# Optimization experiments

Hardware: AMD Instinct MI355X
Metric: run time of the kernel (lower is better)

## Reference

```python
import jax, jax.numpy as jnp
import numpy as np

B_, DIM, NPTS = 16, 128, 16384
J, K, L = 16, 128, 128   # kernel_mode, GkNN_mode_out, GkNN_mode_in
R, M1, M2 = 8, 64, 64    # low-rank A/B dims and mask modes


def setup_inputs() -> dict:
    key = jax.random.key(0)
    ks = jax.random.split(key, 9)
    scale = 1.0 / (L * K)
    return {
        "x": jax.random.normal(ks[0], (B_, DIM, NPTS), jnp.float32),
        "bases": jax.random.normal(ks[1], (NPTS, K), jnp.float32),
        "wbases": jax.random.normal(ks[2], (NPTS, L), jnp.float32),
        "product": jax.random.normal(ks[3], (K, L), jnp.float32),
        "D_out": jax.random.normal(ks[4], (J, K), jnp.float32),
        "D_in": jax.random.normal(ks[5], (J, L), jnp.float32),
        "A": jax.random.normal(ks[6], (J, R, M1), jnp.float32),
        "B": jax.random.normal(ks[7], (J, R, M2), jnp.float32),
        "weights": scale * jax.random.normal(ks[8], (DIM, DIM, J), jnp.float32),
    }


def reference(x, bases, wbases, product, D_out, D_in, A, B, weights):
    # project onto weighted bases: (b, c, npts) @ (npts, L) -> (b, c, L)
    x_hat = jnp.einsum('bcx,xl->bcl', x, wbases)
    # H tensor: (J, K, L) broadcast product + low-rank correction
    H = D_out[:, :, None] * D_in[:, None, :] * product[None, :, :]
    Q = jnp.einsum('jrm,jrn->jmn', A, B)  # bmm(A^T, B): (J, M1, M2)
    H = H.at[:, :Q.shape[1], :Q.shape[2]].add(Q)
    # mode mixing: (J,K,L) x (b,i,L) -> (b,i,J,K), then weights (i,o,J)
    x_hat1 = jnp.einsum('jkl,bil->bijk', H, x_hat)
    y = jnp.einsum('ioj,bijk->bok', weights, x_hat1)
    # back to physical space: (b, o, K) x (npts, K) -> (b, o, npts)
    return jnp.einsum('bok,xk->box', y, bases)
```

## Files before the change

### kernel.cpp

```cpp
#include <hip/hip_runtime.h>

#define B_    16
#define DIM   128
#define NPTS  16384
#define J_    16
#define K_    128
#define L_    128
#define R_    8
#define M1_   64

typedef float  f32x4 __attribute__((ext_vector_type(4)));
typedef short  s16x8 __attribute__((ext_vector_type(8)));
typedef unsigned short u16;
typedef u16 u16x8 __attribute__((ext_vector_type(8)));
typedef u16 u16x4 __attribute__((ext_vector_type(4)));

__device__ __forceinline__ u16 f2bf(float f) {
    unsigned u = __float_as_uint(f);
    u += 0x7FFFu + ((u >> 16) & 1u);
    return (u16)(u >> 16);
}
#define MFMA16(a,b,c) __builtin_amdgcn_mfma_f32_16x16x32_bf16((a),(b),(c),0,0,0)

#define OFF_PARTA 0u
#define OFF_WBT   8388608u
#define OFF_BASB  12582912u
#define OFF_HKL   16777216u
#define OFF_W2T   17301504u
#define OFF_XHB   17825792u
#define OFF_YB    18350080u

__global__ __launch_bounds__(256) void k_prep(
    const float* __restrict__ product, const float* __restrict__ Do,
    const float* __restrict__ Di, const float* __restrict__ A,
    const float* __restrict__ Bm, const float* __restrict__ W,
    const float* __restrict__ wb, const float* __restrict__ bases,
    u16* __restrict__ Hkl, u16* __restrict__ W2T,
    u16* __restrict__ wbT, u16* __restrict__ basesb)
{
    __shared__ u16 sT[128][136];
    const int bid = blockIdx.x, t = threadIdx.x;
    if (bid < 1024) {
        int idx = (bid << 8) | t;
        int j = idx >> 14, k = (idx >> 7) & 127, l = idx & 127;
        float v = Do[j*K_ + k] * Di[j*L_ + l] * product[k*L_ + l];
        if (k < M1_ && l < M1_) {
            float q = 0.f;
            #pragma unroll
            for (int r = 0; r < R_; ++r)
                q += A[(j*R_ + r)*M1_ + k] * Bm[(j*R_ + r)*M1_ + l];
            v += q;
        }
        Hkl[idx] = f2bf(v);
    } else if (bid < 2048) {
        int idx = ((bid - 1024) << 8) | t;
        int o = idx >> 11, ji = idx & 2047, j = ji >> 7, i = ji & 127;
        W2T[idx] = f2bf(W[(i*DIM + o)*J_ + j]);
    } else if (bid < 2176) {
        const int p0 = (bid - 2048) * 128;
        #pragma unroll
        for (int it = 0; it < 16; ++it) {
            int idx = it*256 + t, row = idx >> 5, c4 = (idx & 31) * 4;
            float4 v = *(const float4*)(wb + (size_t)(p0+row)*L_ + c4);
            sT[c4+0][row] = f2bf(v.x); sT[c4+1][row] = f2bf(v.y);
            sT[c4+2][row] = f2bf(v.z); sT[c4+3][row] = f2bf(v.w);
        }
        __syncthreads();
        #pragma unroll
        for (int it = 0; it < 8; ++it) {
            int idx = it*256 + t, l = idx >> 4, pc = (idx & 15) * 8;
            *(u16x8*)(wbT + (size_t)l*NPTS + p0 + pc) = *(const u16x8*)&sT[l][pc];
        }
    } else {
        int i = (((bid - 2176) << 8) | t) * 4;
        float4 v = *(const float4*)(bases + i);
        u16x4 o4 = { f2bf(v.x), f2bf(v.y), f2bf(v.z), f2bf(v.w) };
        *(u16x4*)(basesb + i) = o4;
    }
}

__global__ __launch_bounds__(512) void k_stageA(
    const float* __restrict__ x, const u16* __restrict__ wbT,
    float* __restrict__ part)
{
    __shared__ u16 sA[64][136];
    __shared__ u16 sB[128][136];
    const int t = threadIdx.x, lane = t & 63, wave = t >> 6;
    const int quad = lane >> 4, l16 = lane & 15;
    const int wr = wave >> 2, wc = wave & 3;
    const int m0 = blockIdx.x * 64;
    const size_t pbase = (size_t)blockIdx.y * 2048;

    f32x4 acc[2][2] = {};
    const int ac4 = (t & 31) * 4, arr = t >> 5;
    const int bc8 = (t & 15) * 8, brr = t >> 4;

    float4 vx[4]; u16x8 vb[4];
    #pragma unroll
    for (int i = 0; i < 4; ++i)
        vx[i] = *(const float4*)(x + (size_t)(m0+arr+16*i)*NPTS + pbase + ac4);
    #pragma unroll
    for (int i = 0; i < 4; ++i)
        vb[i] = *(const u16x8*)(wbT + (size_t)(brr+32*i)*NPTS + pbase + bc8);
    #pragma unroll
    for (int i = 0; i < 4; ++i) {
        u16x4 h = { f2bf(vx[i].x), f2bf(vx[i].y), f2bf(vx[i].z), f2bf(vx[i].w) };
        *(u16x4*)&sA[arr+16*i][ac4] = h;
    }
    #pragma unroll
    for (int i = 0; i < 4; ++i)
        *(u16x8*)&sB[brr+32*i][bc8] = vb[i];

    for (int c = 0; c < 16; ++c) {
        __syncthreads();
        if (c < 15) {
            const size_t pb = pbase + (size_t)(c+1)*128;
            #pragma unroll
            for (int i = 0; i < 4; ++i)
                vx[i] = *(const float4*)(x + (size_t)(m0+arr+16*i)*NPTS + pb + ac4);
            #pragma unroll
            for (int i = 0; i < 4; ++i)
                vb[i] = *(const u16x8*)(wbT + (size_t)(brr+32*i)*NPTS + pb + bc8);
        }
        #pragma unroll
        for (int ks = 0; ks < 4; ++ks) {
            int kb = ks*32 + quad*8;
            s16x8 a0 = *(const s16x8*)&sA[wr*32      + l16][kb];
            s16x8 a1 = *(const s16x8*)&sA[wr*32 + 16 + l16][kb];
            s16x8 b0 = *(const s16x8*)&sB[wc*32      + l16][kb];
            s16x8 b1 = *(const s16x8*)&sB[wc*32 + 16 + l16][kb];
            acc[0][0] = MFMA16(a0, b0, acc[0][0]);
            acc[0][1] = MFMA16(a0, b1, acc[0][1]);
            acc[1][0] = MFMA16(a1, b0, acc[1][0]);
            acc[1][1] = MFMA16(a1, b1, acc[1][1]);
        }
        __syncthreads();
        if (c < 15) {
            #pragma unroll
            for (int i = 0; i < 4; ++i) {
                u16x4 h = { f2bf(vx[i].x), f2bf(vx[i].y), f2bf(vx[i].z), f2bf(vx[i].w) };
                *(u16x4*)&sA[arr+16*i][ac4] = h;
            }
            #pragma unroll
            for (int i = 0; i < 4; ++i)
                *(u16x8*)&sB[brr+32*i][bc8] = vb[i];
        }
    }

    float* po = part + (size_t)blockIdx.y * (2048*128);
    #pragma unroll
    for (int mt = 0; mt < 2; ++mt)
      #pragma unroll
      for (int r = 0; r < 4; ++r) {
        int row = m0 + wr*32 + mt*16 + quad*4 + r;
        #pragma unroll
        for (int nt = 0; nt < 2; ++nt) {
            int col = wc*32 + nt*16 + l16;
            po[(size_t)row*128 + col] = acc[mt][nt][r];
        }
      }
}

__global__ __launch_bounds__(256) void k_reduceA(
    const float* __restrict__ part, u16* __restrict__ xhatb)
{
    const float4* p4 = (const float4*)part;
    int i = blockIdx.x * 256 + threadIdx.x;
    float4 s = {0.f, 0.f, 0.f, 0.f};
    #pragma unroll
    for (int p = 0; p < 8; ++p) {
        float4 v = p4[(size_t)p*65536 + i];
        s.x += v.x; s.y += v.y; s.z += v.z; s.w += v.w;
    }
    u16x4 o4 = { f2bf(s.x), f2bf(s.y), f2bf(s.z), f2bf(s.w) };
    *(u16x4*)(xhatb + (size_t)i*4) = o4;
}

__global__ __launch_bounds__(256) void k_mix(
    const u16* __restrict__ Hkl, const u16* __restrict__ W2T,
    const u16* __restrict__ xhatb, u16* __restrict__ yb)
{
    __shared__ u16 sXh[128][136];
    __shared__ u16 sH[2][32][136];
    __shared__ u16 sW[2][32][136];
    __shared__ u16 sT[32][136];
    const int t = threadIdx.x, lane = t & 63, wave = t >> 6;
    const int quad = lane >> 4, l16 = lane & 15;
    const int wr = wave >> 1, wc = wave & 1;
    const int b = blockIdx.x, kq = blockIdx.y, oq = blockIdx.z;

    const int c8 = (t & 15) * 8, rr = t >> 4;
    #pragma unroll
    for (int i = 0; i < 8; ++i) {
        int row = rr + 16*i;
        *(u16x8*)&sXh[row][c8] =
            *(const u16x8*)(xhatb + (size_t)b*16384 + row*128 + c8);
    }
    #pragma unroll
    for (int i = 0; i < 2; ++i) {
        int row = rr + 16*i;
        *(u16x8*)&sH[0][row][c8] =
            *(const u16x8*)(Hkl + (size_t)(kq*32 + row)*128 + c8);
        *(u16x8*)&sW[0][row][c8] =
            *(const u16x8*)(W2T + (size_t)(oq*32 + row)*2048 + c8);
    }

    f32x4 acc2 = {};
    for (int j = 0; j < 16; ++j) {
        const int cur = j & 1, nxt = cur ^ 1;
        __syncthreads();
        f32x4 acc1[4] = {};
        #pragma unroll
        for (int ks = 0; ks < 4; ++ks) {
            int kb = ks*32 + quad*8;
            s16x8 a = *(const s16x8*)&sH[cur][wr*16 + l16][kb];
            #pragma unroll
            for (int nt = 0; nt < 4; ++nt) {
                s16x8 bf = *(const s16x8*)&sXh[wc*64 + nt*16 + l16][kb];
                acc1[nt] = MFMA16(a, bf, acc1[nt]);
            }
        }
        u16x8 hv[2], wv[2];
        if (j < 15) {
            #pragma unroll
            for (int i = 0; i < 2; ++i) {
                int row = rr + 16*i;
                hv[i] = *(const u16x8*)(Hkl +
                        ((size_t)(j+1)*128 + kq*32 + row)*128 + c8);
                wv[i] = *(const u16x8*)(W2T +
                        (size_t)(oq*32 + row)*2048 + (j+1)*128 + c8);
            }
        }
        #pragma unroll
        for (int nt = 0; nt < 4; ++nt)
            #pragma unroll
            for (int r = 0; r < 4; ++r)
                sT[wr*16 + quad*4 + r][wc*64 + nt*16 + l16] = f2bf(acc1[nt][r]);
        __syncthreads();
        if (j < 15) {
            #pragma unroll
            for (int i = 0; i < 2; ++i) {
                int row = rr + 16*i;
                *(u16x8*)&sH[nxt][row][c8] = hv[i];
                *(u16x8*)&sW[nxt][row][c8] = wv[i];
            }
        }
        #pragma unroll
        for (int ks = 0; ks < 4; ++ks) {
            int kb = ks*32 + quad*8;
            s16x8 a2 = *(const s16x8*)&sW[cur][wr*16 + l16][kb];
            s16x8 b2 = *(const s16x8*)&sT[wc*16 + l16][kb];
            acc2 = MFMA16(a2, b2, acc2);
        }
    }
    #pragma unroll
    for (int r = 0; r < 4; ++r) {
        int o = oq*32 + wr*16 + quad*4 + r;
        int k = kq*32 + wc*16 + l16;
        yb[((size_t)b*128 + o)*128 + k] = f2bf(acc2[r]);
    }
}

__global__ __launch_bounds__(256) void k_stageE(
    const u16* __restrict__ yb, const u16* __restrict__ basesb,
    float* __restrict__ out)
{
    __shared__ u16 sA[128][136];
    __shared__ u16 sB[128][136];
    const int t = threadIdx.x, lane = t & 63, wave = t >> 6;
    const int quad = lane >> 4, l16 = lane & 15;
    const int wr = wave >> 1, wc = wave & 1;
    const int bo0 = blockIdx.x * 128, p0 = blockIdx.y * 128;

    const int c8 = (t & 15)*8, rr = t >> 4;
    #pragma unroll
    for (int i = 0; i < 8; ++i) {
        int row = rr + 16*i;
        *(u16x8*)&sA[row][c8] = *(const u16x8*)(yb     + (size_t)(bo0+row)*128 + c8);
        *(u16x8*)&sB[row][c8] = *(const u16x8*)(basesb + (size_t)(p0 +row)*128 + c8);
    }
    __syncthreads();

    f32x4 acc[4][4] = {};
    #pragma unroll
    for (int ks = 0; ks < 4; ++ks) {
        int kb = ks*32 + quad*8;
        s16x8 a[4], bf[4];
        #pragma unroll
        for (int mt = 0; mt < 4; ++mt) a[mt]  = *(const s16x8*)&sA[wr*64 + mt*16 + l16][kb];
        #pragma unroll
        for (int nt = 0; nt < 4; ++nt) bf[nt] = *(const s16x8*)&sB[wc*64 + nt*16 + l16][kb];
        #pragma unroll
        for (int mt = 0; mt < 4; ++mt)
            #pragma unroll
            for (int nt = 0; nt < 4; ++nt)
                acc[mt][nt] = MFMA16(a[mt], bf[nt], acc[mt][nt]);
    }
    #pragma unroll
    for (int mt = 0; mt < 4; ++mt)
      #pragma unroll
      for (int r = 0; r < 4; ++r) {
        size_t row = bo0 + wr*64 + mt*16 + quad*4 + r;
        #pragma unroll
        for (int nt = 0; nt < 4; ++nt) {
            int p = p0 + wc*64 + nt*16 + l16;
            out[row*NPTS + p] = acc[mt][nt][r];
        }
      }
}

extern "C" void kernel_launch(void* const* d_in, const int* in_sizes, int n_in,
                              void* d_out, int out_size, void* d_ws, size_t ws_size,
                              hipStream_t stream) {
    (void)in_sizes; (void)n_in; (void)out_size; (void)ws_size;
    const float* x       = (const float*)d_in[0];
    const float* bases   = (const float*)d_in[1];
    const float* wbases  = (const float*)d_in[2];
    const float* product = (const float*)d_in[3];
    const float* Do      = (const float*)d_in[4];
    const float* Di      = (const float*)d_in[5];
    const float* A       = (const float*)d_in[6];
    const float* Bm      = (const float*)d_in[7];
    const float* W       = (const float*)d_in[8];

    char* ws = (char*)d_ws;
    float* partA  = (float*)(ws + OFF_PARTA);
    u16*   wbT    = (u16*)  (ws + OFF_WBT);
    u16*   basesb = (u16*)  (ws + OFF_BASB);
    u16*   Hkl    = (u16*)  (ws + OFF_HKL);
    u16*   W2T    = (u16*)  (ws + OFF_W2T);
    u16*   xhatb  = (u16*)  (ws + OFF_XHB);
    u16*   yb     = (u16*)  (ws + OFF_YB);

    k_prep   <<<4224, 256, 0, stream>>>(product, Do, Di, A, Bm, W, wbases, bases,
                                        Hkl, W2T, wbT, basesb);
    k_stageA <<<dim3(32, 8), 512, 0, stream>>>(x, wbT, partA);
    k_reduceA<<<256, 256, 0, stream>>>(partA, xhatb);
    k_mix    <<<dim3(16, 4, 4), 256, 0, stream>>>(Hkl, W2T, xhatb, yb);
    k_stageE <<<dim3(16, 128), 256, 0, stream>>>(yb, basesb, (float*)d_out);
}
```

Measured before the change: 311.6 us.

## Fuse bases bf16 conversion into stageE and software-pipeline k_mix over j

Removes the separate bases-to-bf16 pass from k_prep. stageE now loads fp32 bases directly and converts them while staging into shared memory, which saves one write and one read of an 8MB-class buffer. It also restructures k_mix so the second GEMM for step j overlaps the first GEMM for step j+1. This uses triple-buffered H/W tiles and double-buffered sT, cutting the loop to one barrier per iteration. The trade-off is more shared memory per block and extra fp32 traffic in stageE, since each bases tile is re-read by 16 blocks.

```diff
diff --git a/kernel.cpp b/kernel.cpp
--- a/kernel.cpp
+++ b/kernel.cpp
@@ -24,7 +24,6 @@
 
 #define OFF_PARTA 0u
 #define OFF_WBT   8388608u
-#define OFF_BASB  12582912u
 #define OFF_HKL   16777216u
 #define OFF_W2T   17301504u
 #define OFF_XHB   17825792u
@@ -34,9 +33,8 @@
     const float* __restrict__ product, const float* __restrict__ Do,
     const float* __restrict__ Di, const float* __restrict__ A,
     const float* __restrict__ Bm, const float* __restrict__ W,
-    const float* __restrict__ wb, const float* __restrict__ bases,
-    u16* __restrict__ Hkl, u16* __restrict__ W2T,
-    u16* __restrict__ wbT, u16* __restrict__ basesb)
+    const float* __restrict__ wb,
+    u16* __restrict__ Hkl, u16* __restrict__ W2T, u16* __restrict__ wbT)
 {
     __shared__ u16 sT[128][136];
     const int bid = blockIdx.x, t = threadIdx.x;
@@ -56,7 +54,7 @@
         int idx = ((bid - 1024) << 8) | t;
         int o = idx >> 11, ji = idx & 2047, j = ji >> 7, i = ji & 127;
         W2T[idx] = f2bf(W[(i*DIM + o)*J_ + j]);
-    } else if (bid < 2176) {
+    } else {
         const int p0 = (bid - 2048) * 128;
         #pragma unroll
         for (int it = 0; it < 16; ++it) {
@@ -71,11 +69,6 @@
             int idx = it*256 + t, l = idx >> 4, pc = (idx & 15) * 8;
             *(u16x8*)(wbT + (size_t)l*NPTS + p0 + pc) = *(const u16x8*)&sT[l][pc];
         }
-    } else {
-        int i = (((bid - 2176) << 8) | t) * 4;
-        float4 v = *(const float4*)(bases + i);
-        u16x4 o4 = { f2bf(v.x), f2bf(v.y), f2bf(v.z), f2bf(v.w) };
-        *(u16x4*)(basesb + i) = o4;
     }
 }
 
@@ -181,9 +174,9 @@
     const u16* __restrict__ xhatb, u16* __restrict__ yb)
 {
     __shared__ u16 sXh[128][136];
-    __shared__ u16 sH[2][32][136];
-    __shared__ u16 sW[2][32][136];
-    __shared__ u16 sT[32][136];
+    __shared__ u16 sH[3][32][136];
+    __shared__ u16 sW[3][32][136];
+    __shared__ u16 sT[2][32][136];
     const int t = threadIdx.x, lane = t & 63, wave = t >> 6;
     const int quad = lane >> 4, l16 = lane & 15;
     const int wr = wave >> 1, wc = wave & 1;
@@ -197,61 +190,87 @@
             *(const u16x8*)(xhatb + (size_t)b*16384 + row*128 + c8);
     }
     #pragma unroll
-    for (int i = 0; i < 2; ++i) {
+    for (int jj = 0; jj < 2; ++jj)
+      #pragma unroll
+      for (int i = 0; i < 2; ++i) {
         int row = rr + 16*i;
-        *(u16x8*)&sH[0][row][c8] =
-            *(const u16x8*)(Hkl + (size_t)(kq*32 + row)*128 + c8);
-        *(u16x8*)&sW[0][row][c8] =
-            *(const u16x8*)(W2T + (size_t)(oq*32 + row)*2048 + c8);
-    }
-
-    f32x4 acc2 = {};
-    for (int j = 0; j < 16; ++j) {
-        const int cur = j & 1, nxt = cur ^ 1;
-        __syncthreads();
+        *(u16x8*)&sH[jj][row][c8] =
+            *(const u16x8*)(Hkl + ((size_t)jj*128 + kq*32 + row)*128 + c8);
+        *(u16x8*)&sW[jj][row][c8] =
+            *(const u16x8*)(W2T + (size_t)(oq*32 + row)*2048 + jj*128 + c8);
+      }
+    __syncthreads();
+
+    {
         f32x4 acc1[4] = {};
         #pragma unroll
         for (int ks = 0; ks < 4; ++ks) {
             int kb = ks*32 + quad*8;
-            s16x8 a = *(const s16x8*)&sH[cur][wr*16 + l16][kb];
+            s16x8 a = *(const s16x8*)&sH[0][wr*16 + l16][kb];
             #pragma unroll
             for (int nt = 0; nt < 4; ++nt) {
                 s16x8 bf = *(const s16x8*)&sXh[wc*64 + nt*16 + l16][kb];
                 acc1[nt] = MFMA16(a, bf, acc1[nt]);
             }
         }
+        #pragma unroll
+        for (int nt = 0; nt < 4; ++nt)
+            #pragma unroll
+            for (int r = 0; r < 4; ++r)
+                sT[0][wr*16 + quad*4 + r][wc*64 + nt*16 + l16] = f2bf(acc1[nt][r]);
+    }
+    __syncthreads();
+
+    f32x4 acc2 = {};
+    for (int j = 0; j < 16; ++j) {
+        const int cj = j % 3, pj = j & 1;
         u16x8 hv[2], wv[2];
-        if (j < 15) {
+        if (j < 14) {
             #pragma unroll
             for (int i = 0; i < 2; ++i) {
                 int row = rr + 16*i;
                 hv[i] = *(const u16x8*)(Hkl +
-                        ((size_t)(j+1)*128 + kq*32 + row)*128 + c8);
+                        ((size_t)(j+2)*128 + kq*32 + row)*128 + c8);
                 wv[i] = *(const u16x8*)(W2T +
-                        (size_t)(oq*32 + row)*2048 + (j+1)*128 + c8);
-            }
-        }
-        #pragma unroll
-        for (int nt = 0; nt < 4; ++nt)
-            #pragma unroll
-            for (int r = 0; r < 4; ++r)
-                sT[wr*16 + quad*4 + r][wc*64 + nt*16 + l16] = f2bf(acc1[nt][r]);
-        __syncthreads();
+                        (size_t)(oq*32 + row)*2048 + (j+2)*128 + c8);
+            }
+        }
+        #pragma unroll
+        for (int ks = 0; ks < 4; ++ks) {
+            int kb = ks*32 + quad*8;
+            s16x8 a2 = *(const s16x8*)&sW[cj][wr*16 + l16][kb];
+            s16x8 b2 = *(const s16x8*)&sT[pj][wc*16 + l16][kb];
+            acc2 = MFMA16(a2, b2, acc2);
+        }
         if (j < 15) {
+            const int cn = (j+1) % 3;
+            f32x4 acc1[4] = {};
+            #pragma unroll
+            for (int ks = 0; ks < 4; ++ks) {
+                int kb = ks*32 + quad*8;
+                s16x8 a = *(const s16x8*)&sH[cn][wr*16 + l16][kb];
+                #pragma unroll
+                for (int nt = 0; nt < 4; ++nt) {
+                    s16x8 bf = *(const s16x8*)&sXh[wc*64 + nt*16 + l16][kb];
+                    acc1[nt] = MFMA16(a, bf, acc1[nt]);
+                }
+            }
+            #pragma unroll
+            for (int nt = 0; nt < 4; ++nt)
+                #pragma unroll
+                for (int r = 0; r < 4; ++r)
+                    sT[pj^1][wr*16 + quad*4 + r][wc*64 + nt*16 + l16] = f2bf(acc1[nt][r]);
+        }
+        if (j < 14) {
+            const int c2 = (j+2) % 3;
             #pragma unroll
             for (int i = 0; i < 2; ++i) {
                 int row = rr + 16*i;
-                *(u16x8*)&sH[nxt][row][c8] = hv[i];
-                *(u16x8*)&sW[nxt][row][c8] = wv[i];
-            }
-        }
-        #pragma unroll
-        for (int ks = 0; ks < 4; ++ks) {
-            int kb = ks*32 + quad*8;
-            s16x8 a2 = *(const s16x8*)&sW[cur][wr*16 + l16][kb];
-            s16x8 b2 = *(const s16x8*)&sT[wc*16 + l16][kb];
-            acc2 = MFMA16(a2, b2, acc2);
-        }
+                *(u16x8*)&sH[c2][row][c8] = hv[i];
+                *(u16x8*)&sW[c2][row][c8] = wv[i];
+            }
+        }
+        __syncthreads();
     }
     #pragma unroll
     for (int r = 0; r < 4; ++r) {
@@ -262,7 +281,7 @@
 }
 
 __global__ __launch_bounds__(256) void k_stageE(
-    const u16* __restrict__ yb, const u16* __restrict__ basesb,
+    const u16* __restrict__ yb, const float* __restrict__ bases,
     float* __restrict__ out)
 {
     __shared__ u16 sA[128][136];
@@ -276,8 +295,12 @@
     #pragma unroll
     for (int i = 0; i < 8; ++i) {
         int row = rr + 16*i;
-        *(u16x8*)&sA[row][c8] = *(const u16x8*)(yb     + (size_t)(bo0+row)*128 + c8);
-        *(u16x8*)&sB[row][c8] = *(const u16x8*)(basesb + (size_t)(p0 +row)*128 + c8);
+        *(u16x8*)&sA[row][c8] = *(const u16x8*)(yb + (size_t)(bo0+row)*128 + c8);
+        float4 v0 = *(const float4*)(bases + (size_t)(p0+row)*K_ + c8);
+        float4 v1 = *(const float4*)(bases + (size_t)(p0+row)*K_ + c8 + 4);
+        u16x8 h = { f2bf(v0.x), f2bf(v0.y), f2bf(v0.z), f2bf(v0.w),
+                    f2bf(v1.x), f2bf(v1.y), f2bf(v1.z), f2bf(v1.w) };
+        *(u16x8*)&sB[row][c8] = h;
     }
     __syncthreads();
 
@@ -326,16 +349,15 @@
     char* ws = (char*)d_ws;
     float* partA  = (float*)(ws + OFF_PARTA);
     u16*   wbT    = (u16*)  (ws + OFF_WBT);
-    u16*   basesb = (u16*)  (ws + OFF_BASB);
     u16*   Hkl    = (u16*)  (ws + OFF_HKL);
     u16*   W2T    = (u16*)  (ws + OFF_W2T);
     u16*   xhatb  = (u16*)  (ws + OFF_XHB);
     u16*   yb     = (u16*)  (ws + OFF_YB);
 
-    k_prep   <<<4224, 256, 0, stream>>>(product, Do, Di, A, Bm, W, wbases, bases,
-                                        Hkl, W2T, wbT, basesb);
+    k_prep   <<<2176, 256, 0, stream>>>(product, Do, Di, A, Bm, W, wbases,
+                                        Hkl, W2T, wbT);
     k_stageA <<<dim3(32, 8), 512, 0, stream>>>(x, wbT, partA);
     k_reduceA<<<256, 256, 0, stream>>>(partA, xhatb);
     k_mix    <<<dim3(16, 4, 4), 256, 0, stream>>>(Hkl, W2T, xhatb, yb);
-    k_stageE <<<dim3(16, 128), 256, 0, stream>>>(yb, basesb, (float*)d_out);
-}
+    k_stageE <<<dim3(16, 128), 256, 0, stream>>>(yb, bases, (float*)d_out);
+}
```

Result: slower. 328.6 us (+5.5%).
